# Kernel tuning notes

Hardware: AMD Instinct MI355X
Metric: run time of the kernel (lower is better)

Reference implementation:

```python
import jax, jax.numpy as jnp
import numpy as np

B, OBS, L, D, BINS, HID = 4096, 128, 4, 8, 16, 512
S = L * D  # max_seq_len = 32; qchunk_size = S, single Q chunk


def _lin(k, i, o, s):
    kw, kb = jax.random.split(k)
    return jax.random.normal(kw, (i, o), jnp.float32) * s, jnp.zeros((o,), jnp.float32)


def setup_inputs() -> dict:
    key = jax.random.key(0)
    ks = jax.random.split(key, 12)
    inp = {
        "obs": jax.random.normal(ks[0], (B, OBS), jnp.float32),
        "category": jax.random.randint(ks[1], (B, L, D), 0, BINS, jnp.int32),
    }
    # v_network: obs_dim -> 512 -> 512 -> 512 -> 1 (tanh hidden)
    dims_v = [OBS, HID, HID, HID, 1]
    for i in range(4):
        w, b = _lin(ks[2 + i], dims_v[i], dims_v[i + 1], 0.05)
        inp[f"v_w{i}"], inp[f"v_b{i}"] = w, b
    # q_network: (obs_dim+actor_dim) -> 512 -> 512 -> 512 -> bins*S
    dims_q = [OBS + D, HID, HID, HID, BINS * S]
    for i in range(4):
        w, b = _lin(ks[6 + i], dims_q[i], dims_q[i + 1], 0.05)
        inp[f"q_w{i}"], inp[f"q_b{i}"] = w, b
    return inp


def _mlp(x, ws, bs):
    for w, b in zip(ws[:-1], bs[:-1]):
        x = jnp.tanh(x @ w + b)
    return x @ ws[-1] + bs[-1]


def _actions_from_category(category):
    # zoom_in per (level, dim): width_l = 2/bins^(l+1); low accumulates cat*width.
    cat = category.astype(jnp.float32)  # (B, L, D)
    widths = 2.0 / (jnp.float32(BINS) ** jnp.arange(1, L + 1, dtype=jnp.float32))  # (L,)
    cum_low = jnp.cumsum(cat * widths[None, :, None], axis=1)  # (B, L, D)
    mids = -1.0 + cum_low + 0.5 * widths[None, :, None]  # midpoint after each level
    # mids_full[:, j, d] = midpoint of dim d after j zoom-in updates (j=0 -> 0.0)
    mids_full = jnp.concatenate(
        [jnp.zeros((category.shape[0], 1, D), jnp.float32), mids], axis=1)  # (B, L+1, D)
    # at sequence step k (input to Q), dim d' has had U[k,d'] updates
    k = jnp.arange(S)
    U = k[:, None] // D + (jnp.arange(D)[None, :] < (k[:, None] % D)).astype(jnp.int32)  # (S, D)
    dgrid = jnp.broadcast_to(jnp.arange(D)[None, :], (S, D))
    return mids_full[:, U, dgrid]  # (B, S, D)


def reference(obs, category,
              v_w0, v_b0, v_w1, v_b1, v_w2, v_b2, v_w3, v_b3,
              q_w0, q_b0, q_w1, q_b1, q_w2, q_b2, q_w3, q_b3):
    vw = [v_w0, v_w1, v_w2, v_w3]; vb = [v_b0, v_b1, v_b2, v_b3]
    qw = [q_w0, q_w1, q_w2, q_w3]; qb = [q_b0, q_b1, q_b2, q_b3]
    b = obs.shape[0]
    actions = _actions_from_category(category)  # (B, S, D)
    obs_rep = jnp.broadcast_to(obs[:, None, :], (b, S, OBS))
    x = jnp.concatenate([obs_rep, actions], axis=-1)  # (B, S, OBS+D)
    adv = _mlp(x, qw, qb)  # (B, S, S*BINS)
    adv = adv.reshape(b, S, S, BINS)
    s_idx = jnp.arange(S)
    adv = adv[:, s_idx, s_idx, :]  # diagonal gather -> (B, S, BINS)
    adv = adv.reshape(b, L, D, BINS)
    value = _mlp(obs, vw, vb)  # (B, 1)
    nbias = jnp.zeros((b, L, D, 1), jnp.float32)  # use_nbias=False
    return value, adv, nbias
```

## Files before the change

kernel.cpp:

```cpp
#include <hip/hip_runtime.h>
#include <hip/hip_bf16.h>

#define B_SZ   4096
#define OBS_N  128
#define HID    512
#define TANH_SCALE 2.885390081777927f


typedef __bf16 bf16x8_t __attribute__((ext_vector_type(8)));
typedef float  f32x4_t  __attribute__((ext_vector_type(4)));

__device__ inline float fast_tanh(float x) {
    float e = __builtin_amdgcn_exp2f(x * TANH_SCALE);
    return fmaf(-2.f, __builtin_amdgcn_rcpf(e + 1.f), 1.f);
}

__device__ inline float fast_tanh_pre(float x) {
    float e = __builtin_amdgcn_exp2f(x);
    return fmaf(-2.f, __builtin_amdgcn_rcpf(e + 1.f), 1.f);
}

__device__ inline void gld_lds16(const void* g, void* l) {
    __builtin_amdgcn_global_load_lds(
        (const __attribute__((address_space(1))) void*)g,
        (__attribute__((address_space(3))) void*)l, 16, 0, 0);
}

__device__ inline int hs_off(int row, int col) {
    int c = col >> 3;
    int phys = (c & ~7) | ((c ^ (row & 7)) & 7);
    return row * 512 + phys * 8 + (col & 7);
}

__global__ __launch_bounds__(256) void prep_kernel(
    const float* __restrict__ obs, const int* __restrict__ category,
    const float* __restrict__ qw0, const float* __restrict__ qb0,
    const float* __restrict__ qw1, const float* __restrict__ qw2,
    const float* __restrict__ qw3,
    const float* __restrict__ vw0, const float* __restrict__ vb0,
    const float* __restrict__ vw1, const float* __restrict__ vw2,
    const float* __restrict__ qb1, const float* __restrict__ qb2,
    const float* __restrict__ vb1, const float* __restrict__ vb2,
    __hip_bfloat16* __restrict__ obs_bf,
    __hip_bfloat16* __restrict__ w0t, __hip_bfloat16* __restrict__ w1t,
    __hip_bfloat16* __restrict__ w2t, __hip_bfloat16* __restrict__ w3t,
    __hip_bfloat16* __restrict__ vw0t, __hip_bfloat16* __restrict__ vw1t,
    __hip_bfloat16* __restrict__ vw2t,
    __hip_bfloat16* __restrict__ w0aug, __hip_bfloat16* __restrict__ vw0aug,
    __hip_bfloat16* __restrict__ acts_bf, float* __restrict__ bias_s,
    float* __restrict__ nbias)
{
    const int bid = blockIdx.x, tid = threadIdx.x;
    if (bid < 2048) {
        int i = bid * 256 + tid;
        obs_bf[i] = __float2bfloat16(obs[i]);
    } else if (bid < 2560) {
        const float* src = (bid < 2304) ? qw0 : vw0;
        __hip_bfloat16* dst = (bid < 2304) ? w0t : vw0t;
        int idx = ((bid - 2048) & 255) * 256 + tid;
        int n = idx >> 7, k = idx & 127;
        dst[idx] = __float2bfloat16(src[k * 512 + n] * TANH_SCALE);
    } else if (bid < 7680) {
        int job = (bid - 2560) >> 10;
        const float* srcs[5] = {qw1, qw2, qw3, vw1, vw2};
        __hip_bfloat16* dsts[5] = {w1t, w2t, w3t, vw1t, vw2t};
        float sc = (job == 2) ? 1.0f : TANH_SCALE;
        int idx = ((bid - 2560) & 1023) * 256 + tid;
        int e    = idx & 7;
        int lane = (idx >> 3) & 63;
        int tile, kc;
        if (job == 2) {
            kc   = (idx >> 9) & 15;
            tile = idx >> 13;
        } else {
            int jj = (idx >> 9) & 3;
            kc     = (idx >> 11) & 15;
            int g  = idx >> 15;
            tile = g * 4 + jj;
        }
        int k = kc * 32 + (lane >> 4) * 8 + e;
        int n = tile * 16 + (lane & 15);
        dsts[job][idx] = __float2bfloat16(srcs[job][k * 512 + n] * sc);
    } else if (bid < 11776) {
        int t = (bid - 7680) * 256 + tid;
        int d = t & 7;
        int r = t >> 3;
        int b = r & 4095, s = r >> 12;
        int U = (s >> 3) + ((d < (s & 7)) ? 1 : 0);
        float a = 0.f;
        if (U > 0) {
            float w = 0.125f, cum = 0.f;
            for (int j = 0; j < U; ++j) {
                cum += (float)category[b * 32 + j * 8 + d] * w;
                if (j == U - 1) a = -1.f + cum + 0.5f * w;
                w *= 0.0625f;
            }
        }
        acts_bf[t] = __float2bfloat16(a);
    } else if (bid < 11904) {
        int sub = bid - 11776;
        bool isv = sub >= 64;
        int idx = (sub & 63) * 256 + tid;
        int e    = idx & 7;
        int lane = (idx >> 3) & 63;
        int tile = idx >> 9;
        int k = (lane >> 4) * 8 + e;
        int n = tile * 16 + (lane & 15);
        float v = 0.f;
        if (!isv) {
            if (k < 8) v = qw0[(128 + k) * 512 + n];
            else if (k == 8) v = qb0[n];
            w0aug[idx] = __float2bfloat16(v * TANH_SCALE);
        } else {
            if (k == 8) v = vb0[n];
            vw0aug[idx] = __float2bfloat16(v * TANH_SCALE);
        }
    } else if (bid < 11912) {
        int idx = (bid - 11904) * 256 + tid;
        const float* srcs[4] = {qb1, qb2, vb1, vb2};
        bias_s[idx] = srcs[idx >> 9][idx & 511] * TANH_SCALE;
    } else {
        int i = (bid - 11912) * 256 + tid;
        nbias[i] = 0.f;
    }
}

__global__ __launch_bounds__(256) void gemm_dual(
    const __hip_bfloat16* __restrict__ A0, const __hip_bfloat16* __restrict__ B0,
    const float* __restrict__ bias0, void* __restrict__ C0, int K0, int epi0, int nb0,
    const __hip_bfloat16* __restrict__ A1, const __hip_bfloat16* __restrict__ B1,
    const float* __restrict__ bias1, void* __restrict__ C1, int K1, int epi1)
{
    __shared__ __hip_bfloat16 As[128 * 32];
    __shared__ __hip_bfloat16 Bs[128 * 32];

    const __hip_bfloat16 *A, *Bt;
    const float* bias;
    void* Cout;
    int K, epi, tb;
    if ((int)blockIdx.x < nb0) {
        A = A0; Bt = B0; bias = bias0; Cout = C0; K = K0; epi = epi0; tb = blockIdx.x;
    } else {
        A = A1; Bt = B1; bias = bias1; Cout = C1; K = K1; epi = epi1; tb = blockIdx.x - nb0;
    }
    const long m0 = (long)(tb >> 2) * 128;
    const int  n0 = (tb & 3) * 128;

    const int tid  = threadIdx.x;
    const int wave = tid >> 6, lane = tid & 63;
    const int quad = lane >> 4, t = lane & 15;
    const int wr = wave >> 1, wc = wave & 1;

    f32x4_t acc[4][4] = {};

    const int lrow  = lane >> 2;
    const int lkoff = (((lane & 3) + (lane >> 3)) & 3) * 8;

    const __hip_bfloat16* Ag0 = A  + (m0 + wave * 32 +      lrow) * (long)K + lkoff;
    const __hip_bfloat16* Ag1 = A  + (m0 + wave * 32 + 16 + lrow) * (long)K + lkoff;
    const __hip_bfloat16* Bg0 = Bt + (long)(n0 + wave * 32 +      lrow) * K + lkoff;
    const __hip_bfloat16* Bg1 = Bt + (long)(n0 + wave * 32 + 16 + lrow) * K + lkoff;
    __hip_bfloat16* AsB0 = &As[(wave * 32) * 32];
    __hip_bfloat16* AsB1 = &As[(wave * 32 + 16) * 32];
    __hip_bfloat16* BsB0 = &Bs[(wave * 32) * 32];
    __hip_bfloat16* BsB1 = &Bs[(wave * 32 + 16) * 32];

    const int slot = ((quad - (t >> 1)) & 3) * 8;

    for (int k0 = 0; k0 < K; k0 += 32) {
        gld_lds16(Ag0 + k0, AsB0);
        gld_lds16(Ag1 + k0, AsB1);
        gld_lds16(Bg0 + k0, BsB0);
        gld_lds16(Bg1 + k0, BsB1);
        __syncthreads();
        bf16x8_t af[4], bfr[4];
        #pragma unroll
        for (int i = 0; i < 4; ++i)
            af[i] = *(const bf16x8_t*)&As[(wr * 64 + i * 16 + t) * 32 + slot];
        #pragma unroll
        for (int j = 0; j < 4; ++j)
            bfr[j] = *(const bf16x8_t*)&Bs[(wc * 64 + j * 16 + t) * 32 + slot];
        #pragma unroll
        for (int i = 0; i < 4; ++i)
            #pragma unroll
            for (int j = 0; j < 4; ++j)
                acc[i][j] = __builtin_amdgcn_mfma_f32_16x16x32_bf16(af[i], bfr[j], acc[i][j], 0, 0, 0);
        __syncthreads();
    }

    #pragma unroll
    for (int i = 0; i < 4; ++i) {
        const long rbase = m0 + wr * 64 + i * 16 + quad * 4;
        #pragma unroll
        for (int j = 0; j < 4; ++j) {
            const int col = n0 + wc * 64 + j * 16 + t;
            #pragma unroll
            for (int r = 0; r < 4; ++r) {
                float v = acc[i][j][r];
                if (epi == 1) {
                    v = fast_tanh(v + bias[col]);
                    ((__hip_bfloat16*)Cout)[(rbase + r) * 512 + col] = __float2bfloat16(v);
                } else if (epi == 2) {
                    ((__hip_bfloat16*)Cout)[(rbase + r) * 512 + col] = __float2bfloat16(v);
                } else if (epi == 3) {
                    const long m = rbase + r;
                    const int brow = (int)(m & 63);
                    const long idx =
                        ((((m >> 6) * 8 + (col >> 6)) * 16 + (brow >> 4) * 4 + ((col >> 4) & 3)) * 256)
                        + ((col >> 2) & 3) * 64 + (brow & 15) * 4 + (col & 3);
                    ((float*)Cout)[idx] = v;
                } else {
                    ((float*)Cout)[(rbase + r) * 512 + col] = v;
                }
            }
        }
    }
}

__device__ inline void epi_store(
    __hip_bfloat16* hs, f32x4_t acc[4][4],
    int n0w, int quad, int t)
{
    #pragma unroll
    for (int j = 0; j < 4; ++j) {
        const int oc0 = n0w + j * 16 + quad * 4;
        const int cbase = oc0 >> 3;
        const int sub = (quad & 1) * 4;
        #pragma unroll
        for (int rt = 0; rt < 4; ++rt) {
            const int row = rt * 16 + t;
            union { __hip_bfloat16 b[4]; uint2 v; } o;
            o.b[0] = __float2bfloat16(fast_tanh_pre(acc[rt][j][0]));
            o.b[1] = __float2bfloat16(fast_tanh_pre(acc[rt][j][1]));
            o.b[2] = __float2bfloat16(fast_tanh_pre(acc[rt][j][2]));
            o.b[3] = __float2bfloat16(fast_tanh_pre(acc[rt][j][3]));
            const int phys = (cbase & ~7) | ((cbase ^ (row & 7)) & 7);
            *(uint2*)&hs[row * 512 + phys * 8 + sub] = o.v;
        }
    }
}

__device__ inline void mfma_layer(
    __hip_bfloat16* hs, const __hip_bfloat16* __restrict__ Wt,
    const float* __restrict__ bias_s, int w, int lane)
{
    const int quad = lane >> 4, t = lane & 15;
    const int n0w = w * 64;
    const __hip_bfloat16* Wl = Wt + (size_t)w * 32768 + (size_t)lane * 8;
    f32x4_t acc[4][4];
    #pragma unroll
    for (int j = 0; j < 4; ++j) {
        const f32x4_t bv = *(const f32x4_t*)&bias_s[n0w + j * 16 + quad * 4];
        #pragma unroll
        for (int rt = 0; rt < 4; ++rt)
            acc[rt][j] = bv;
    }
    bf16x8_t wA[4], wB[4], ac[4];
    #pragma unroll
    for (int j = 0; j < 4; ++j) {
        wA[j] = *(const bf16x8_t*)(Wl + (size_t)(0 * 4 + j) * 512);
        wB[j] = *(const bf16x8_t*)(Wl + (size_t)(1 * 4 + j) * 512);
    }

    for (int m = 0; m < 8; ++m) {
        {
            const int kc = 2 * m;
            const int craw = kc * 4 + quad;
            const int phys = (craw & ~7) | ((craw ^ (t & 7)) & 7);
            #pragma unroll
            for (int rt = 0; rt < 4; ++rt)
                ac[rt] = *(const bf16x8_t*)&hs[(rt * 16 + t) * 512 + phys * 8];
            __builtin_amdgcn_s_setprio(1);
            #pragma unroll
            for (int j = 0; j < 4; ++j)
                #pragma unroll
                for (int rt = 0; rt < 4; ++rt)
                    acc[rt][j] = __builtin_amdgcn_mfma_f32_16x16x32_bf16(wA[j], ac[rt], acc[rt][j], 0, 0, 0);
            __builtin_amdgcn_s_setprio(0);
            if (m < 7) {
                #pragma unroll
                for (int j = 0; j < 4; ++j)
                    wA[j] = *(const bf16x8_t*)(Wl + (size_t)((kc + 2) * 4 + j) * 512);
            }
        }
        {
            const int kc = 2 * m + 1;
            const int craw = kc * 4 + quad;
            const int phys = (craw & ~7) | ((craw ^ (t & 7)) & 7);
            #pragma unroll
            for (int rt = 0; rt < 4; ++rt)
                ac[rt] = *(const bf16x8_t*)&hs[(rt * 16 + t) * 512 + phys * 8];
            __builtin_amdgcn_s_setprio(1);
            #pragma unroll
            for (int j = 0; j < 4; ++j)
                #pragma unroll
                for (int rt = 0; rt < 4; ++rt)
                    acc[rt][j] = __builtin_amdgcn_mfma_f32_16x16x32_bf16(wB[j], ac[rt], acc[rt][j], 0, 0, 0);
            __builtin_amdgcn_s_setprio(0);
            if (m < 7) {
                #pragma unroll
                for (int j = 0; j < 4; ++j)
                    wB[j] = *(const bf16x8_t*)(Wl + (size_t)((kc + 2) * 4 + j) * 512);
            }
        }
    }
    __syncthreads();
    epi_store(hs, acc, n0w, quad, t);
    __syncthreads();
}

__global__ __launch_bounds__(512, 4) void fused_kernel(
    const float* __restrict__ p,
    const float* __restrict__ pv,
    const __hip_bfloat16* __restrict__ acts_bf,
    const __hip_bfloat16* __restrict__ w0aug,
    const __hip_bfloat16* __restrict__ vw0aug,
    const __hip_bfloat16* __restrict__ w1t, const float* __restrict__ qb1s,
    const __hip_bfloat16* __restrict__ w2t, const float* __restrict__ qb2s,
    const __hip_bfloat16* __restrict__ w3t, const float* __restrict__ qb3,
    float* __restrict__ advout,
    const __hip_bfloat16* __restrict__ vw1t, const float* __restrict__ vb1s,
    const __hip_bfloat16* __restrict__ vw2t, const float* __restrict__ vb2s,
    const float* __restrict__ vw3, const float* __restrict__ vb3,
    float* __restrict__ vout)
{
    __shared__ __hip_bfloat16 hs[64 * 512];
    const int bid = blockIdx.x;
    const int tid = threadIdx.x;
    const int w = tid >> 6, lane = tid & 63;
    const int quad = lane >> 4, t = lane & 15;
    const bool is_q = bid < 2048;
    const int s  = is_q ? (bid >> 6) : 0;
    const int mb = is_q ? (bid & 63) : (bid - 2048);
    const int n0w = w * 64;

    {
        const float* Pt = (is_q ? p : pv) + (((size_t)mb * 8 + w) * 16) * 256 + lane * 4;
        const __hip_bfloat16* W0 = is_q ? w0aug : vw0aug;
        f32x4_t acc[4][4];
        #pragma unroll
        for (int rt = 0; rt < 4; ++rt)
            #pragma unroll
            for (int j = 0; j < 4; ++j)
                acc[rt][j] = *(const f32x4_t*)(Pt + (rt * 4 + j) * 256);
        bf16x8_t bfrag[4];
        #pragma unroll
        for (int rt = 0; rt < 4; ++rt) {
            union { bf16x8_t vec; unsigned short u[8]; } bu;
            #pragma unroll
            for (int i = 0; i < 8; ++i) bu.u[i] = 0;
            if (quad == 1) bu.u[0] = 0x3F80;
            if (is_q && quad == 0) {
                const long r = (long)s * 4096 + mb * 64 + rt * 16 + t;
                bu.vec = *(const bf16x8_t*)&acts_bf[r * 8];
            }
            bfrag[rt] = bu.vec;
        }
        bf16x8_t wq[4];
        #pragma unroll
        for (int j = 0; j < 4; ++j)
            wq[j] = *(const bf16x8_t*)(W0 + ((size_t)(w * 4 + j) * 64 + lane) * 8);
        __builtin_amdgcn_s_setprio(1);
        #pragma unroll
        for (int j = 0; j < 4; ++j)
            #pragma unroll
            for (int rt = 0; rt < 4; ++rt)
                acc[rt][j] = __builtin_amdgcn_mfma_f32_16x16x32_bf16(wq[j], bfrag[rt], acc[rt][j], 0, 0, 0);
        __builtin_amdgcn_s_setprio(0);
        epi_store(hs, acc, n0w, quad, t);
    }
    __syncthreads();

    mfma_layer(hs, is_q ? w1t : vw1t, is_q ? qb1s : vb1s, w, lane);
    mfma_layer(hs, is_q ? w2t : vw2t, is_q ? qb2s : vb2s, w, lane);

    if (is_q) {
        f32x4_t acc = {};
        if (w < 4) {
            const __hip_bfloat16* W3l = w3t + ((size_t)s * 16 * 64 + (size_t)lane) * 8;
            #pragma unroll 4
            for (int kc = 0; kc < 16; ++kc) {
                const int craw = kc * 4 + quad;
                const int phys = (craw & ~7) | ((craw ^ (t & 7)) & 7);
                bf16x8_t a = *(const bf16x8_t*)&hs[(w * 16 + t) * 512 + phys * 8];
                bf16x8_t bq = *(const bf16x8_t*)(W3l + (size_t)kc * 512);
                acc = __builtin_amdgcn_mfma_f32_16x16x32_bf16(a, bq, acc, 0, 0, 0);
            }
        }
        __syncthreads();
        float* hsf = (float*)hs;
        if (w < 4) {
            const float bias3 = qb3[s * 16 + t];
            #pragma unroll
            for (int rr = 0; rr < 4; ++rr)
                hsf[(w * 16 + quad * 4 + rr) * 16 + t] = acc[rr] + bias3;
        }
        __syncthreads();
        const int row = tid >> 3, cp = tid & 7;
        float2 v2 = *(const float2*)&hsf[row * 16 + cp * 2];
        *(float2*)&advout[(size_t)(mb * 64 + row) * 512 + s * 16 + cp * 2] = v2;
    } else {
        const int row = tid >> 3, seg = tid & 7;
        float sum = 0.f;
        for (int k = seg * 64; k < seg * 64 + 64; ++k)
            sum += __bfloat162float(hs[hs_off(row, k)]) * vw3[k];
        sum += __shfl_xor(sum, 1);
        sum += __shfl_xor(sum, 2);
        sum += __shfl_xor(sum, 4);
        if (seg == 0) vout[mb * 64 + row] = sum + vb3[0];
    }
}

extern "C" void kernel_launch(void* const* d_in, const int* in_sizes, int n_in,
                              void* d_out, int out_size, void* d_ws, size_t ws_size,
                              hipStream_t stream) {
    const float* obs      = (const float*)d_in[0];
    const int*   category = (const int*)d_in[1];
    const float* v_w0 = (const float*)d_in[2];
    const float* v_b0 = (const float*)d_in[3];
    const float* v_w1 = (const float*)d_in[4];
    const float* v_b1 = (const float*)d_in[5];
    const float* v_w2 = (const float*)d_in[6];
    const float* v_b2 = (const float*)d_in[7];
    const float* v_w3 = (const float*)d_in[8];
    const float* v_b3 = (const float*)d_in[9];
    const float* q_w0 = (const float*)d_in[10];
    const float* q_b0 = (const float*)d_in[11];
    const float* q_w1 = (const float*)d_in[12];
    const float* q_b1 = (const float*)d_in[13];
    const float* q_w2 = (const float*)d_in[14];
    const float* q_b2 = (const float*)d_in[15];
    const float* q_w3 = (const float*)d_in[16];
    const float* q_b3 = (const float*)d_in[17];

    char* ws = (char*)d_ws;
    __hip_bfloat16* obs_bf = (__hip_bfloat16*)(ws + 0);
    __hip_bfloat16* w0t    = (__hip_bfloat16*)(ws + 1048576);
    __hip_bfloat16* vw0t   = (__hip_bfloat16*)(ws + 1179648);
    __hip_bfloat16* w1t    = (__hip_bfloat16*)(ws + 1310720);
    __hip_bfloat16* w2t    = (__hip_bfloat16*)(ws + 1835008);
    __hip_bfloat16* w3t    = (__hip_bfloat16*)(ws + 2359296);
    __hip_bfloat16* vw1t   = (__hip_bfloat16*)(ws + 2883584);
    __hip_bfloat16* vw2t   = (__hip_bfloat16*)(ws + 3407872);
    __hip_bfloat16* w0aug  = (__hip_bfloat16*)(ws + 3932160);
    __hip_bfloat16* vw0aug = (__hip_bfloat16*)(ws + 3964928);
    __hip_bfloat16* acts_bf= (__hip_bfloat16*)(ws + 3997696);
    float*          p      = (float*)         (ws + 6094848);
    float*          pv     = (float*)         (ws + 14483456);
    float*          bias_s = (float*)         (ws + 22872064);

    float* out       = (float*)d_out;
    float* out_value = out;
    float* out_adv   = out + 4096;
    float* out_nbias = out + 4096 + (size_t)B_SZ * 512;

    prep_kernel<<<12424, 256, 0, stream>>>(
        obs, category, q_w0, q_b0, q_w1, q_w2, q_w3, v_w0, v_b0, v_w1, v_w2,
        q_b1, q_b2, v_b1, v_b2,
        obs_bf, w0t, w1t, w2t, w3t, vw0t, vw1t, vw2t, w0aug, vw0aug,
        acts_bf, bias_s, out_nbias);

    gemm_dual<<<256, 256, 0, stream>>>(
        obs_bf, w0t, nullptr, p, 128, 3, 128,
        obs_bf, vw0t, nullptr, pv, 128, 3);

    fused_kernel<<<2112, 512, 0, stream>>>(
        p, pv, acts_bf, w0aug, vw0aug,
        w1t, bias_s, w2t, bias_s + 512, w3t, q_b3, out_adv,
        vw1t, bias_s + 1024, vw2t, bias_s + 1536, v_w3, v_b3, out_value);
}
```

Baseline: 255.9 us.

## Triple-buffer weight prefetch in MFMA layer loop and vectorize prep kernel copies

The inner MFMA layer now rotates through three weight register buffers instead of two, so each global weight load is issued two k-chunks ahead. The goal is to hide more global-load latency behind MFMA work. The loop is restructured into a templated k-chunk body with the tail peeled, and it is kept rolled with `#pragma unroll 1`. Separately, the prep kernel converts obs and zeroes nbias with float4 accesses, which cuts the block count; in exchange the MFMA path uses more registers, which may pressure occupancy under launch_bounds(512,4).

```diff
diff --git a/kernel.cpp b/kernel.cpp
--- a/kernel.cpp
+++ b/kernel.cpp
@@ -51,21 +51,27 @@
     float* __restrict__ nbias)
 {
     const int bid = blockIdx.x, tid = threadIdx.x;
-    if (bid < 2048) {
-        int i = bid * 256 + tid;
-        obs_bf[i] = __float2bfloat16(obs[i]);
-    } else if (bid < 2560) {
-        const float* src = (bid < 2304) ? qw0 : vw0;
-        __hip_bfloat16* dst = (bid < 2304) ? w0t : vw0t;
-        int idx = ((bid - 2048) & 255) * 256 + tid;
+    if (bid < 512) {
+        int i = bid * 1024 + tid * 4;
+        float4 v = *(const float4*)&obs[i];
+        union { __hip_bfloat16 b[4]; uint2 u; } o;
+        o.b[0] = __float2bfloat16(v.x);
+        o.b[1] = __float2bfloat16(v.y);
+        o.b[2] = __float2bfloat16(v.z);
+        o.b[3] = __float2bfloat16(v.w);
+        *(uint2*)&obs_bf[i] = o.u;
+    } else if (bid < 1024) {
+        const float* src = (bid < 768) ? qw0 : vw0;
+        __hip_bfloat16* dst = (bid < 768) ? w0t : vw0t;
+        int idx = ((bid - 512) & 255) * 256 + tid;
         int n = idx >> 7, k = idx & 127;
         dst[idx] = __float2bfloat16(src[k * 512 + n] * TANH_SCALE);
-    } else if (bid < 7680) {
-        int job = (bid - 2560) >> 10;
+    } else if (bid < 6144) {
+        int job = (bid - 1024) >> 10;
         const float* srcs[5] = {qw1, qw2, qw3, vw1, vw2};
         __hip_bfloat16* dsts[5] = {w1t, w2t, w3t, vw1t, vw2t};
         float sc = (job == 2) ? 1.0f : TANH_SCALE;
-        int idx = ((bid - 2560) & 1023) * 256 + tid;
+        int idx = ((bid - 1024) & 1023) * 256 + tid;
         int e    = idx & 7;
         int lane = (idx >> 3) & 63;
         int tile, kc;
@@ -81,8 +87,8 @@
         int k = kc * 32 + (lane >> 4) * 8 + e;
         int n = tile * 16 + (lane & 15);
         dsts[job][idx] = __float2bfloat16(srcs[job][k * 512 + n] * sc);
-    } else if (bid < 11776) {
-        int t = (bid - 7680) * 256 + tid;
+    } else if (bid < 10240) {
+        int t = (bid - 6144) * 256 + tid;
         int d = t & 7;
         int r = t >> 3;
         int b = r & 4095, s = r >> 12;
@@ -97,8 +103,8 @@
             }
         }
         acts_bf[t] = __float2bfloat16(a);
-    } else if (bid < 11904) {
-        int sub = bid - 11776;
+    } else if (bid < 10368) {
+        int sub = bid - 10240;
         bool isv = sub >= 64;
         int idx = (sub & 63) * 256 + tid;
         int e    = idx & 7;
@@ -115,13 +121,14 @@
             if (k == 8) v = vb0[n];
             vw0aug[idx] = __float2bfloat16(v * TANH_SCALE);
         }
-    } else if (bid < 11912) {
-        int idx = (bid - 11904) * 256 + tid;
+    } else if (bid < 10376) {
+        int idx = (bid - 10368) * 256 + tid;
         const float* srcs[4] = {qb1, qb2, vb1, vb2};
         bias_s[idx] = srcs[idx >> 9][idx & 511] * TANH_SCALE;
     } else {
-        int i = (bid - 11912) * 256 + tid;
-        nbias[i] = 0.f;
+        int i = (bid - 10376) * 1024 + tid * 4;
+        float4 z = {0.f, 0.f, 0.f, 0.f};
+        *(float4*)&nbias[i] = z;
     }
 }
 
@@ -240,6 +247,35 @@
     }
 }
 
+template<bool DO_PRE>
+__device__ inline void kc_body(
+    const __hip_bfloat16* hs, const __hip_bfloat16* __restrict__ Wl,
+    bf16x8_t (&ws)[4], f32x4_t (&acc)[4][4],
+    int kc_use, int kc_pre, int quad, int t)
+{
+    const int craw = kc_use * 4 + quad;
+    const int phys = (craw & ~7) | ((craw ^ (t & 7)) & 7);
+    const __hip_bfloat16* hrow = &hs[t * 512 + phys * 8];
+    bf16x8_t a0 = *(const bf16x8_t*)(hrow + 0 * 8192);
+    bf16x8_t a1 = *(const bf16x8_t*)(hrow + 1 * 8192);
+    bf16x8_t a2 = *(const bf16x8_t*)(hrow + 2 * 8192);
+    bf16x8_t a3 = *(const bf16x8_t*)(hrow + 3 * 8192);
+    __builtin_amdgcn_s_setprio(1);
+    #pragma unroll
+    for (int j = 0; j < 4; ++j) {
+        acc[0][j] = __builtin_amdgcn_mfma_f32_16x16x32_bf16(ws[j], a0, acc[0][j], 0, 0, 0);
+        acc[1][j] = __builtin_amdgcn_mfma_f32_16x16x32_bf16(ws[j], a1, acc[1][j], 0, 0, 0);
+        acc[2][j] = __builtin_amdgcn_mfma_f32_16x16x32_bf16(ws[j], a2, acc[2][j], 0, 0, 0);
+        acc[3][j] = __builtin_amdgcn_mfma_f32_16x16x32_bf16(ws[j], a3, acc[3][j], 0, 0, 0);
+    }
+    __builtin_amdgcn_s_setprio(0);
+    if (DO_PRE) {
+        #pragma unroll
+        for (int j = 0; j < 4; ++j)
+            ws[j] = *(const bf16x8_t*)(Wl + (size_t)(kc_pre * 4 + j) * 512);
+    }
+}
+
 __device__ inline void mfma_layer(
     __hip_bfloat16* hs, const __hip_bfloat16* __restrict__ Wt,
     const float* __restrict__ bias_s, int w, int lane)
@@ -255,55 +291,25 @@
         for (int rt = 0; rt < 4; ++rt)
             acc[rt][j] = bv;
     }
-    bf16x8_t wA[4], wB[4], ac[4];
+    bf16x8_t wA[4], wB[4], wC[4];
     #pragma unroll
     for (int j = 0; j < 4; ++j) {
         wA[j] = *(const bf16x8_t*)(Wl + (size_t)(0 * 4 + j) * 512);
         wB[j] = *(const bf16x8_t*)(Wl + (size_t)(1 * 4 + j) * 512);
-    }
-
-    for (int m = 0; m < 8; ++m) {
-        {
-            const int kc = 2 * m;
-            const int craw = kc * 4 + quad;
-            const int phys = (craw & ~7) | ((craw ^ (t & 7)) & 7);
-            #pragma unroll
-            for (int rt = 0; rt < 4; ++rt)
-                ac[rt] = *(const bf16x8_t*)&hs[(rt * 16 + t) * 512 + phys * 8];
-            __builtin_amdgcn_s_setprio(1);
-            #pragma unroll
-            for (int j = 0; j < 4; ++j)
-                #pragma unroll
-                for (int rt = 0; rt < 4; ++rt)
-                    acc[rt][j] = __builtin_amdgcn_mfma_f32_16x16x32_bf16(wA[j], ac[rt], acc[rt][j], 0, 0, 0);
-            __builtin_amdgcn_s_setprio(0);
-            if (m < 7) {
-                #pragma unroll
-                for (int j = 0; j < 4; ++j)
-                    wA[j] = *(const bf16x8_t*)(Wl + (size_t)((kc + 2) * 4 + j) * 512);
-            }
-        }
-        {
-            const int kc = 2 * m + 1;
-            const int craw = kc * 4 + quad;
-            const int phys = (craw & ~7) | ((craw ^ (t & 7)) & 7);
-            #pragma unroll
-            for (int rt = 0; rt < 4; ++rt)
-                ac[rt] = *(const bf16x8_t*)&hs[(rt * 16 + t) * 512 + phys * 8];
-            __builtin_amdgcn_s_setprio(1);
-            #pragma unroll
-            for (int j = 0; j < 4; ++j)
-                #pragma unroll
-                for (int rt = 0; rt < 4; ++rt)
-                    acc[rt][j] = __builtin_amdgcn_mfma_f32_16x16x32_bf16(wB[j], ac[rt], acc[rt][j], 0, 0, 0);
-            __builtin_amdgcn_s_setprio(0);
-            if (m < 7) {
-                #pragma unroll
-                for (int j = 0; j < 4; ++j)
-                    wB[j] = *(const bf16x8_t*)(Wl + (size_t)((kc + 2) * 4 + j) * 512);
-            }
-        }
-    }
+        wC[j] = *(const bf16x8_t*)(Wl + (size_t)(2 * 4 + j) * 512);
+    }
+
+    #pragma unroll 1
+    for (int m = 0; m < 4; ++m) {
+        kc_body<true>(hs, Wl, wA, acc, 3 * m,     3 * m + 3, quad, t);
+        kc_body<true>(hs, Wl, wB, acc, 3 * m + 1, 3 * m + 4, quad, t);
+        kc_body<true>(hs, Wl, wC, acc, 3 * m + 2, 3 * m + 5, quad, t);
+    }
+    kc_body<true >(hs, Wl, wA, acc, 12, 15, quad, t);
+    kc_body<false>(hs, Wl, wB, acc, 13, 0, quad, t);
+    kc_body<false>(hs, Wl, wC, acc, 14, 0, quad, t);
+    kc_body<false>(hs, Wl, wA, acc, 15, 0, quad, t);
+
     __syncthreads();
     epi_store(hs, acc, n0w, quad, t);
     __syncthreads();
@@ -454,7 +460,7 @@
     float* out_adv   = out + 4096;
     float* out_nbias = out + 4096 + (size_t)B_SZ * 512;
 
-    prep_kernel<<<12424, 256, 0, stream>>>(
+    prep_kernel<<<10504, 256, 0, stream>>>(
         obs, category, q_w0, q_b0, q_w1, q_w2, q_w3, v_w0, v_b0, v_w1, v_w2,
         q_b1, q_b2, v_b1, v_b2,
         obs_bf, w0t, w1t, w2t, w3t, vw0t, vw1t, vw2t, w0aug, vw0aug,
```

Result: slower. 399.1 us (+56.0%).
